# Optimization experiments

Measured on AMD Instinct MI355X. Metric: run time of the kernel, lower is better.

The kernel has to match this reference:

```python
import jax, jax.numpy as jnp
import numpy as np


def setup_inputs() -> dict:
    key = jax.random.key(0)
    ks = jax.random.split(key, 5)
    B, S, D, U = 4, 2048, 1024, 1024
    scale = 1.0 / np.sqrt(D)
    return {
        "query": jax.random.normal(ks[0], (B, S, D), dtype=jnp.float32),
        "value": jax.random.normal(ks[1], (B, S, D), dtype=jnp.float32),
        "Wq": jax.random.normal(ks[2], (D, U), dtype=jnp.float32) * scale,
        "bq": jnp.zeros((U,), dtype=jnp.float32),
        "Wk": jax.random.normal(ks[3], (D, U), dtype=jnp.float32) * scale,
        "bk": jnp.zeros((U,), dtype=jnp.float32),
        "Wv": jax.random.normal(ks[4], (D, U), dtype=jnp.float32) * scale,
        "bv": jnp.zeros((U,), dtype=jnp.float32),
    }


def reference(query, value, Wq, bq, Wk, bk, Wv, bv):
    # Dense projections (last-dim matmul + bias)
    Q = jnp.einsum("bsd,du->bsu", query, Wq) + bq   # [B,Sq,U]
    K = jnp.einsum("btd,du->btu", value, Wk) + bk   # [B,Sk,U]
    V = jnp.einsum("btd,du->btu", value, Wv) + bv   # [B,Sk,U]
    d_k = jnp.asarray(K.shape[-1], dtype=jnp.float32)
    scores = jnp.einsum("bsu,btu->bst", Q, K) / jnp.sqrt(d_k)  # [B,Sq,Sk]
    weights = jax.nn.softmax(scores, axis=-1)
    return jnp.einsum("bst,btu->bsu", weights, V)   # [B,Sq,U]
```

## Files before the change

kernel.cpp:

```cpp
#include <hip/hip_runtime.h>
#include <hip/hip_bf16.h>
#include <stdint.h>

#define DEVINL __device__ __forceinline__

typedef __attribute__((ext_vector_type(4))) float f32x4;
typedef __attribute__((ext_vector_type(8))) __bf16 bfv8;
typedef __attribute__((ext_vector_type(8))) short s16x8;
typedef __attribute__((ext_vector_type(4))) short s16x4;

DEVINL short f2bf(float f) {
  union { float f; unsigned u; } v; v.f = f;
  unsigned r = v.u + 0x7FFFu + ((v.u >> 16) & 1u);
  return (short)(r >> 16);
}
DEVINL float bf2f(short h) {
  union { unsigned u; float f; } v; v.u = ((unsigned)(unsigned short)h) << 16;
  return v.f;
}
DEVINL void gload_lds16(const void* g, void* l) {
  __builtin_amdgcn_global_load_lds((__attribute__((address_space(1))) unsigned*)(g),
                                   (__attribute__((address_space(3))) unsigned*)(l),
                                   16, 0, 0);
}
#define S_BARRIER() __builtin_amdgcn_s_barrier()
#define LGKM0() asm volatile("s_waitcnt lgkmcnt(0)" ::: "memory")
#define MEMORD() asm volatile("" ::: "memory")
template <int N> DEVINL void vmwaitc() {
  asm volatile("s_waitcnt vmcnt(%0)" :: "i"(N) : "memory");
}
DEVINL int xswz(int p, int n) { return (p & 7) * (n >> 3) + (p >> 3); }

template <int BU, int NF, int RING>
DEVINL void gemm_core(const short* __restrict__ Ag, const short* __restrict__ Bg,
                      int lda, int ldb, int m0, int n0, int nkt,
                      short* lds, f32x4 (&acc)[8][NF]) {
  constexpr int U = 2 + BU;
  constexpr int SLOT = 8192 + BU * 4096;
  constexpr int WS = (RING - 2) * U;
  const int tid = threadIdx.x;
  const int w = tid >> 6, l = tid & 63;
  const int wm = w >> 2, wn = w & 3;
  const int lr = l & 15, lg = l >> 4;
  const int stg_row = w * 16 + (l >> 2);
  const int stg_col = (((l & 3) ^ ((l >> 3) & 3)) << 3);
  const int ck = ((lg ^ ((lr >> 1) & 3)) << 3);
  const int aro = (wm * 128 + lr) * 32 + ck;
  const int bro = 8192 + (wn * (NF * 16) + lr) * 32 + ck;
  const int dW = w * 512;

#pragma unroll
  for (int t = 0; t < RING - 1; ++t) {
    short* S = lds + t * SLOT;
    gload_lds16(Ag + (size_t)(m0 + stg_row) * lda + t * 32 + stg_col, S + dW);
    gload_lds16(Ag + (size_t)(m0 + 128 + stg_row) * lda + t * 32 + stg_col, S + 4096 + dW);
#pragma unroll
    for (int u = 0; u < BU; ++u)
      gload_lds16(Bg + (size_t)(n0 + u * 128 + stg_row) * ldb + t * 32 + stg_col,
                  S + 8192 + u * 4096 + dW);
  }
  vmwaitc<WS>(); S_BARRIER(); MEMORD();

  int cur = 0, stg = RING - 1;
  bfv8 a[4], b[NF];
#pragma unroll 1
  for (int kt = 0; kt < nkt; ++kt) {
    const short* Sc = lds + cur * SLOT;
    short* Ss = lds + stg * SLOT;
    const int ks = kt + (RING - 1);
#pragma unroll
    for (int mf = 0; mf < 4; ++mf) a[mf] = *(const bfv8*)(Sc + aro + mf * 512);
#pragma unroll
    for (int nf = 0; nf < NF; ++nf) b[nf] = *(const bfv8*)(Sc + bro + nf * 512);
    if (ks < nkt) {
      gload_lds16(Ag + (size_t)(m0 + stg_row) * lda + ks * 32 + stg_col, Ss + dW);
      gload_lds16(Ag + (size_t)(m0 + 128 + stg_row) * lda + ks * 32 + stg_col, Ss + 4096 + dW);
    }
    S_BARRIER(); LGKM0();
    __builtin_amdgcn_s_setprio(1);
#pragma unroll
    for (int mf = 0; mf < 4; ++mf)
#pragma unroll
      for (int nf = 0; nf < NF; ++nf)
        acc[mf][nf] = __builtin_amdgcn_mfma_f32_16x16x32_bf16(a[mf], b[nf], acc[mf][nf], 0, 0, 0);
    __builtin_amdgcn_s_setprio(0);
    S_BARRIER(); MEMORD();
#pragma unroll
    for (int mf = 0; mf < 4; ++mf) a[mf] = *(const bfv8*)(Sc + aro + 2048 + mf * 512);
    if (ks < nkt) {
#pragma unroll
      for (int u = 0; u < BU; ++u)
        gload_lds16(Bg + (size_t)(n0 + u * 128 + stg_row) * ldb + ks * 32 + stg_col,
                    Ss + 8192 + u * 4096 + dW);
    }
    if (kt + 1 < nkt) {
      if (ks < nkt) vmwaitc<WS>();
      else if (kt + 2 < nkt) vmwaitc<U>();
      else vmwaitc<0>();
    }
    S_BARRIER(); LGKM0();
    __builtin_amdgcn_s_setprio(1);
#pragma unroll
    for (int mf = 0; mf < 4; ++mf)
#pragma unroll
      for (int nf = 0; nf < NF; ++nf)
        acc[4 + mf][nf] = __builtin_amdgcn_mfma_f32_16x16x32_bf16(a[mf], b[nf], acc[4 + mf][nf], 0, 0, 0);
    __builtin_amdgcn_s_setprio(0);
    S_BARRIER(); MEMORD();
    cur = (cur + 1 == RING) ? 0 : cur + 1;
    stg = (stg + 1 == RING) ? 0 : stg + 1;
  }
}

__global__ __launch_bounds__(256) void prep_kernel(
    const float* __restrict__ q, const float* __restrict__ v,
    const float* __restrict__ Wq, const float* __restrict__ Wk, const float* __restrict__ Wv,
    short* __restrict__ Qc, short* __restrict__ Vc,
    short* __restrict__ WTq, short* __restrict__ WTk, short* __restrict__ WTv) {
  __shared__ float tile[64][65];
  const int bx = blockIdx.x;
  if (bx < 8192) {
    const float* src = (bx < 4096) ? q : v;
    short* dst = (bx < 4096) ? Qc : Vc;
    const size_t i = ((size_t)(bx & 4095) * 256 + threadIdx.x) * 8;
    f32x4 x0 = *(const f32x4*)(src + i);
    f32x4 x1 = *(const f32x4*)(src + i + 4);
    s16x8 o;
#pragma unroll
    for (int j = 0; j < 4; ++j) { o[j] = f2bf(x0[j]); o[4 + j] = f2bf(x1[j]); }
    *(s16x8*)(dst + i) = o;
  } else {
    const int z = (bx - 8192) >> 8, xx = (bx - 8192) & 255;
    const float* W = (z == 0) ? Wq : (z == 1) ? Wk : Wv;
    short* WT = (z == 0) ? WTq : (z == 1) ? WTk : WTv;
    const int k0 = (xx & 15) << 6, n0 = (xx >> 4) << 6;
    const int c = threadIdx.x & 63, r0 = threadIdx.x >> 6;
#pragma unroll
    for (int i = 0; i < 16; ++i) {
      int r = (i << 2) + r0;
      tile[r][c] = W[(size_t)(k0 + r) * 1024 + n0 + c];
    }
    __syncthreads();
#pragma unroll
    for (int i = 0; i < 16; ++i) {
      int a = (i << 2) + r0;
      WT[(size_t)(n0 + a) * 1024 + k0 + c] = f2bf(tile[c][a]);
    }
  }
}

__global__ __launch_bounds__(512, 4) void qkproj_kernel(
    const short* __restrict__ Qc, const short* __restrict__ Vc,
    const short* __restrict__ WTq, const short* __restrict__ WTk,
    const float* __restrict__ bq, const float* __restrict__ bk,
    short* __restrict__ Qb, short* __restrict__ Kb) {
  __shared__ short lds[36864];
  const int o = xswz(blockIdx.x, 512);
  const int sel = o >> 8, r = o & 255;
  const int bm = r >> 3, bn = r & 7;
  const short* A = sel ? Vc : Qc;
  const short* BT = sel ? WTk : WTq;
  const float* bias = sel ? bk : bq;
  short* O = sel ? Kb : Qb;
  const int m0 = bm * 256, n0 = bn * 128;
  f32x4 acc[8][2];
#pragma unroll
  for (int i = 0; i < 8; ++i)
#pragma unroll
    for (int j = 0; j < 2; ++j) acc[i][j] = (f32x4){0.f, 0.f, 0.f, 0.f};
  gemm_core<1, 2, 3>(A, BT, 1024, 1024, m0, n0, 32, lds, acc);
  const int tid = threadIdx.x;
  const int w = tid >> 6, l = tid & 63;
  const int wm = w >> 2, wn = w & 3, lr = l & 15, lg = l >> 4;
#pragma unroll
  for (int i = 0; i < 8; ++i) {
    const int row0 = m0 + wm * 128 + (i >> 2) * 64 + (i & 3) * 16 + lg * 4;
#pragma unroll
    for (int nf = 0; nf < 2; ++nf) {
      const int col = n0 + wn * 32 + nf * 16 + lr;
      const float bb = bias[col];
#pragma unroll
      for (int j = 0; j < 4; ++j)
        O[(size_t)(row0 + j) * 1024 + col] = f2bf(acc[i][nf][j] + bb);
    }
  }
}

__global__ __launch_bounds__(512, 2) void vproj_kernel(
    const short* __restrict__ Vc, const short* __restrict__ WTv,
    const float* __restrict__ bv, short* __restrict__ VT) {
  __shared__ short lds[36864];
  const int o = xswz(blockIdx.x, 256);
  const int bm = o >> 3, bn = o & 7;
  const int m0 = bm * 256, n0 = bn * 128;
  f32x4 acc[8][2];
#pragma unroll
  for (int i = 0; i < 8; ++i)
#pragma unroll
    for (int j = 0; j < 2; ++j) acc[i][j] = (f32x4){0.f, 0.f, 0.f, 0.f};
  gemm_core<1, 2, 3>(Vc, WTv, 1024, 1024, m0, n0, 32, lds, acc);
  const int tid = threadIdx.x;
  const int w = tid >> 6, l = tid & 63;
  const int wm = w >> 2, wn = w & 3, lr = l & 15, lg = l >> 4;
  __syncthreads();
  short* lt = lds;
#pragma unroll
  for (int i = 0; i < 8; ++i) {
    const int tl = wm * 128 + (i >> 2) * 64 + (i & 3) * 16 + lg * 4;
#pragma unroll
    for (int nf = 0; nf < 2; ++nf) {
      const int ul = wn * 32 + nf * 16 + lr;
      const float bb = bv[n0 + ul];
      s16x4 pk;
#pragma unroll
      for (int j = 0; j < 4; ++j) pk[j] = f2bf(acc[i][nf][j] + bb);
      *(s16x4*)&lt[ul * 264 + tl] = pk;
    }
  }
  __syncthreads();
  const int b = m0 >> 11, t0 = m0 & 2047;
#pragma unroll
  for (int it = 0; it < 8; ++it) {
    const int cid = it * 512 + tid;
    const int u = cid >> 5, tc = cid & 31;
    s16x8 v8 = *(const s16x8*)&lt[u * 264 + tc * 8];
    *(s16x8*)(VT + ((size_t)b * 1024 + n0 + u) * 2048 + t0 + tc * 8) = v8;
  }
}

__global__ __launch_bounds__(512, 4) void qkt_kernel(const short* __restrict__ Qb,
                                                     const short* __restrict__ Kb,
                                                     short* __restrict__ Sb) {
  __shared__ short lds[36864];
  const int o = xswz(blockIdx.x, 512);
  const int bt = o >> 7, r = o & 127;
  const int bm = r >> 4, bn = r & 15;
  const short* A = Qb + (size_t)bt * 2097152;
  const short* B = Kb + (size_t)bt * 2097152;
  short* O = Sb + (size_t)bt * 4194304;
  const int m0 = bm * 256, n0 = bn * 128;
  f32x4 acc[8][2];
#pragma unroll
  for (int i = 0; i < 8; ++i)
#pragma unroll
    for (int j = 0; j < 2; ++j) acc[i][j] = (f32x4){0.f, 0.f, 0.f, 0.f};
  gemm_core<1, 2, 3>(A, B, 1024, 1024, m0, n0, 32, lds, acc);
  const int tid = threadIdx.x;
  const int w = tid >> 6, l = tid & 63;
  const int wm = w >> 2, wn = w & 3, lr = l & 15, lg = l >> 4;
#pragma unroll
  for (int i = 0; i < 8; ++i) {
    const int row0 = m0 + wm * 128 + (i >> 2) * 64 + (i & 3) * 16 + lg * 4;
#pragma unroll
    for (int nf = 0; nf < 2; ++nf) {
      const int col = n0 + wn * 32 + nf * 16 + lr;
#pragma unroll
      for (int j = 0; j < 4; ++j)
        O[(size_t)(row0 + j) * 2048 + col] = f2bf(acc[i][nf][j] * 0.03125f);
    }
  }
}

__global__ __launch_bounds__(512, 2) void pv_kernel(const short* __restrict__ Sb,
                                                    const short* __restrict__ VT,
                                                    float* __restrict__ Out) {
  __shared__ short lds[36864];
  const int o = xswz(blockIdx.x, 256);
  const int bt = o >> 6, r = o & 63;
  const int bm = r >> 3, bn = r & 7;
  const short* A = Sb + (size_t)bt * 4194304;
  const short* B = VT + (size_t)bt * 2097152;
  float* O = Out + (size_t)bt * 2097152;
  const int m0 = bm * 256, n0 = bn * 128;
  f32x4 acc[8][2];
#pragma unroll
  for (int i = 0; i < 8; ++i)
#pragma unroll
    for (int j = 0; j < 2; ++j) acc[i][j] = (f32x4){0.f, 0.f, 0.f, 0.f};
  gemm_core<1, 2, 3>(A, B, 2048, 2048, m0, n0, 64, lds, acc);
  const int l = threadIdx.x & 63, w = threadIdx.x >> 6;
  const int wm = w >> 2, wn = w & 3, lr = l & 15, lg = l >> 4;
#pragma unroll
  for (int i = 0; i < 8; ++i) {
    const int row0 = m0 + wm * 128 + (i >> 2) * 64 + (i & 3) * 16 + lg * 4;
#pragma unroll
    for (int nf = 0; nf < 2; ++nf) {
      const int col = n0 + wn * 32 + nf * 16 + lr;
#pragma unroll
      for (int j = 0; j < 4; ++j)
        O[(size_t)(row0 + j) * 1024 + col] = acc[i][nf][j];
    }
  }
}

__global__ __launch_bounds__(256) void softmax_kernel(short* __restrict__ Sb) {
  const size_t row = blockIdx.x;
  short* p = Sb + row * 2048;
  const int tid = threadIdx.x;
  const int w = tid >> 6, l = tid & 63;
  s16x8 v = *(const s16x8*)(p + tid * 8);
  float f[8];
#pragma unroll
  for (int j = 0; j < 8; ++j) f[j] = bf2f(v[j]);
  float m = f[0];
#pragma unroll
  for (int j = 1; j < 8; ++j) m = fmaxf(m, f[j]);
#pragma unroll
  for (int o = 32; o > 0; o >>= 1) m = fmaxf(m, __shfl_xor(m, o, 64));
  __shared__ float redm[4], reds[4];
  if (l == 0) redm[w] = m;
  __syncthreads();
  m = fmaxf(fmaxf(redm[0], redm[1]), fmaxf(redm[2], redm[3]));
  float s = 0.f;
#pragma unroll
  for (int j = 0; j < 8; ++j) { f[j] = __expf(f[j] - m); s += f[j]; }
#pragma unroll
  for (int o = 32; o > 0; o >>= 1) s += __shfl_xor(s, o, 64);
  if (l == 0) reds[w] = s;
  __syncthreads();
  s = reds[0] + reds[1] + reds[2] + reds[3];
  const float inv = 1.f / s;
  s16x8 o8;
#pragma unroll
  for (int j = 0; j < 8; ++j) o8[j] = f2bf(f[j] * inv);
  *(s16x8*)(p + tid * 8) = o8;
}

extern "C" void kernel_launch(void* const* d_in, const int* in_sizes, int n_in,
                              void* d_out, int out_size, void* d_ws, size_t ws_size,
                              hipStream_t stream) {
  const float* query = (const float*)d_in[0];
  const float* value = (const float*)d_in[1];
  const float* Wq = (const float*)d_in[2];
  const float* bq = (const float*)d_in[3];
  const float* Wk = (const float*)d_in[4];
  const float* bk = (const float*)d_in[5];
  const float* Wv = (const float*)d_in[6];
  const float* bv = (const float*)d_in[7];

  char* ws = (char*)d_ws;
  short* WTq = (short*)(ws);
  short* WTk = (short*)(ws + ((size_t)2 << 20));
  short* WTv = (short*)(ws + ((size_t)4 << 20));
  short* Qc  = (short*)(ws + ((size_t)6 << 20));
  short* Vc  = (short*)(ws + ((size_t)22 << 20));
  short* Sb  = (short*)(ws + ((size_t)6 << 20));
  short* Qb  = (short*)(ws + ((size_t)38 << 20));
  short* Kb  = (short*)(ws + ((size_t)54 << 20));
  short* VT  = (short*)(ws + ((size_t)70 << 20));

  prep_kernel<<<dim3(8960), 256, 0, stream>>>(query, value, Wq, Wk, Wv, Qc, Vc, WTq, WTk, WTv);

  qkproj_kernel<<<dim3(512), 512, 0, stream>>>(Qc, Vc, WTq, WTk, bq, bk, Qb, Kb);
  vproj_kernel<<<dim3(256), 512, 0, stream>>>(Vc, WTv, bv, VT);

  qkt_kernel<<<dim3(512), 512, 0, stream>>>(Qb, Kb, Sb);

  softmax_kernel<<<dim3(8192), 256, 0, stream>>>(Sb);

  pv_kernel<<<dim3(256), 512, 0, stream>>>(Sb, VT, (float*)d_out);
}
```

Baseline: 193.0 us.

## Double-buffer LDS fragments in GEMM core to overlap reads with MFMA

Restructures the GEMM main loop to unroll by two k-tiles and keep two register sets of A/B fragments. LDS reads for the next half-tile are issued before the MFMAs of the current one, instead of loading then waiting on lgkmcnt(0). The explicit lgkmcnt waits and setprio calls are dropped, and global-to-LDS staging is spread across the phases with finer vmcnt waits. The extra fragment registers raise register pressure. The loop now assumes nkt is even and that the vmcnt<2> waits line up with the new staging order.

```diff
diff --git a/kernel.cpp b/kernel.cpp
--- a/kernel.cpp
+++ b/kernel.cpp
@@ -24,7 +24,6 @@
                                    16, 0, 0);
 }
 #define S_BARRIER() __builtin_amdgcn_s_barrier()
-#define LGKM0() asm volatile("s_waitcnt lgkmcnt(0)" ::: "memory")
 #define MEMORD() asm volatile("" ::: "memory")
 template <int N> DEVINL void vmwaitc() {
   asm volatile("s_waitcnt vmcnt(%0)" :: "i"(N) : "memory");
@@ -37,7 +36,6 @@
                       short* lds, f32x4 (&acc)[8][NF]) {
   constexpr int U = 2 + BU;
   constexpr int SLOT = 8192 + BU * 4096;
-  constexpr int WS = (RING - 2) * U;
   const int tid = threadIdx.x;
   const int w = tid >> 6, l = tid & 63;
   const int wm = w >> 2, wn = w & 3;
@@ -49,67 +47,81 @@
   const int bro = 8192 + (wn * (NF * 16) + lr) * 32 + ck;
   const int dW = w * 512;
 
-#pragma unroll
-  for (int t = 0; t < RING - 1; ++t) {
-    short* S = lds + t * SLOT;
-    gload_lds16(Ag + (size_t)(m0 + stg_row) * lda + t * 32 + stg_col, S + dW);
-    gload_lds16(Ag + (size_t)(m0 + 128 + stg_row) * lda + t * 32 + stg_col, S + 4096 + dW);
-#pragma unroll
-    for (int u = 0; u < BU; ++u)
-      gload_lds16(Bg + (size_t)(n0 + u * 128 + stg_row) * ldb + t * 32 + stg_col,
-                  S + 8192 + u * 4096 + dW);
-  }
-  vmwaitc<WS>(); S_BARRIER(); MEMORD();
-
-  int cur = 0, stg = RING - 1;
-  bfv8 a[4], b[NF];
+#define STAGE_A(t) { short* S_ = lds + ((t) % RING) * SLOT;                                \
+    gload_lds16(Ag + (size_t)(m0 + stg_row) * lda + (t) * 32 + stg_col, S_ + dW);          \
+    gload_lds16(Ag + (size_t)(m0 + 128 + stg_row) * lda + (t) * 32 + stg_col,              \
+                S_ + 4096 + dW); }
+#define STAGE_B(t) { short* S_ = lds + ((t) % RING) * SLOT;                                \
+    _Pragma("unroll")                                                                      \
+    for (int u_ = 0; u_ < BU; ++u_)                                                        \
+      gload_lds16(Bg + (size_t)(n0 + u_ * 128 + stg_row) * ldb + (t) * 32 + stg_col,       \
+                  S_ + 8192 + u_ * 4096 + dW); }
+
+#pragma unroll
+  for (int t = 0; t < RING - 1; ++t) { STAGE_A(t); STAGE_B(t); }
+  vmwaitc<(RING - 2) * U>(); S_BARRIER(); MEMORD();
+
+  bfv8 aA[4], aB[4], bA[NF], bB[NF];
+  {
+    const short* Sp = lds;
+#pragma unroll
+    for (int mf = 0; mf < 4; ++mf) aA[mf] = *(const bfv8*)(Sp + aro + mf * 512);
+#pragma unroll
+    for (int nf = 0; nf < NF; ++nf) bA[nf] = *(const bfv8*)(Sp + bro + nf * 512);
+  }
+
 #pragma unroll 1
-  for (int kt = 0; kt < nkt; ++kt) {
-    const short* Sc = lds + cur * SLOT;
-    short* Ss = lds + stg * SLOT;
-    const int ks = kt + (RING - 1);
-#pragma unroll
-    for (int mf = 0; mf < 4; ++mf) a[mf] = *(const bfv8*)(Sc + aro + mf * 512);
-#pragma unroll
-    for (int nf = 0; nf < NF; ++nf) b[nf] = *(const bfv8*)(Sc + bro + nf * 512);
-    if (ks < nkt) {
-      gload_lds16(Ag + (size_t)(m0 + stg_row) * lda + ks * 32 + stg_col, Ss + dW);
-      gload_lds16(Ag + (size_t)(m0 + 128 + stg_row) * lda + ks * 32 + stg_col, Ss + 4096 + dW);
-    }
-    S_BARRIER(); LGKM0();
-    __builtin_amdgcn_s_setprio(1);
+  for (int kt = 0; kt < nkt; kt += 2) {
+    const short* S0 = lds + (kt % RING) * SLOT;
+    const short* S1 = lds + ((kt + 1) % RING) * SLOT;
+    const short* S2 = lds + ((kt + 2) % RING) * SLOT;
+    if (kt + 2 < nkt) STAGE_A(kt + 2);
+#pragma unroll
+    for (int mf = 0; mf < 4; ++mf) aB[mf] = *(const bfv8*)(S0 + aro + 2048 + mf * 512);
 #pragma unroll
     for (int mf = 0; mf < 4; ++mf)
 #pragma unroll
       for (int nf = 0; nf < NF; ++nf)
-        acc[mf][nf] = __builtin_amdgcn_mfma_f32_16x16x32_bf16(a[mf], b[nf], acc[mf][nf], 0, 0, 0);
-    __builtin_amdgcn_s_setprio(0);
+        acc[mf][nf] = __builtin_amdgcn_mfma_f32_16x16x32_bf16(aA[mf], bA[nf], acc[mf][nf], 0, 0, 0);
+    if (kt + 2 < nkt) vmwaitc<2>(); else vmwaitc<0>();
     S_BARRIER(); MEMORD();
-#pragma unroll
-    for (int mf = 0; mf < 4; ++mf) a[mf] = *(const bfv8*)(Sc + aro + 2048 + mf * 512);
-    if (ks < nkt) {
-#pragma unroll
-      for (int u = 0; u < BU; ++u)
-        gload_lds16(Bg + (size_t)(n0 + u * 128 + stg_row) * ldb + ks * 32 + stg_col,
-                    Ss + 8192 + u * 4096 + dW);
-    }
-    if (kt + 1 < nkt) {
-      if (ks < nkt) vmwaitc<WS>();
-      else if (kt + 2 < nkt) vmwaitc<U>();
-      else vmwaitc<0>();
-    }
-    S_BARRIER(); LGKM0();
-    __builtin_amdgcn_s_setprio(1);
+    if (kt + 2 < nkt) STAGE_B(kt + 2);
+#pragma unroll
+    for (int mf = 0; mf < 4; ++mf) aA[mf] = *(const bfv8*)(S1 + aro + mf * 512);
+#pragma unroll
+    for (int nf = 0; nf < NF; ++nf) bB[nf] = *(const bfv8*)(S1 + bro + nf * 512);
 #pragma unroll
     for (int mf = 0; mf < 4; ++mf)
 #pragma unroll
       for (int nf = 0; nf < NF; ++nf)
-        acc[4 + mf][nf] = __builtin_amdgcn_mfma_f32_16x16x32_bf16(a[mf], b[nf], acc[4 + mf][nf], 0, 0, 0);
-    __builtin_amdgcn_s_setprio(0);
+        acc[4 + mf][nf] = __builtin_amdgcn_mfma_f32_16x16x32_bf16(aB[mf], bA[nf], acc[4 + mf][nf], 0, 0, 0);
     S_BARRIER(); MEMORD();
-    cur = (cur + 1 == RING) ? 0 : cur + 1;
-    stg = (stg + 1 == RING) ? 0 : stg + 1;
-  }
+    if (kt + 3 < nkt) STAGE_A(kt + 3);
+#pragma unroll
+    for (int mf = 0; mf < 4; ++mf) aB[mf] = *(const bfv8*)(S1 + aro + 2048 + mf * 512);
+#pragma unroll
+    for (int mf = 0; mf < 4; ++mf)
+#pragma unroll
+      for (int nf = 0; nf < NF; ++nf)
+        acc[mf][nf] = __builtin_amdgcn_mfma_f32_16x16x32_bf16(aA[mf], bB[nf], acc[mf][nf], 0, 0, 0);
+    if (kt + 3 < nkt) vmwaitc<2>(); else vmwaitc<0>();
+    S_BARRIER(); MEMORD();
+    if (kt + 3 < nkt) STAGE_B(kt + 3);
+    if (kt + 2 < nkt) {
+#pragma unroll
+      for (int mf = 0; mf < 4; ++mf) aA[mf] = *(const bfv8*)(S2 + aro + mf * 512);
+#pragma unroll
+      for (int nf = 0; nf < NF; ++nf) bA[nf] = *(const bfv8*)(S2 + bro + nf * 512);
+    }
+#pragma unroll
+    for (int mf = 0; mf < 4; ++mf)
+#pragma unroll
+      for (int nf = 0; nf < NF; ++nf)
+        acc[4 + mf][nf] = __builtin_amdgcn_mfma_f32_16x16x32_bf16(aB[mf], bB[nf], acc[4 + mf][nf], 0, 0, 0);
+    S_BARRIER(); MEMORD();
+  }
+#undef STAGE_A
+#undef STAGE_B
 }
 
 __global__ __launch_bounds__(256) void prep_kernel(
```

Measured after the change: 190.2 us. About the same (-1.4%).
